# Kernel optimization log

Measured on AMD Instinct MI355X. Metric: run time of the kernel, lower is better.

The kernel has to match this reference:

```python
import jax, jax.numpy as jnp
import numpy as np

N, C, S = 16, 512, 4096

def setup_inputs() -> dict:
    rng = jax.random.key(0)
    k1, k2, k3 = jax.random.split(rng, 3)
    return {
        "key": jax.random.normal(k1, (N, C, S), dtype=jnp.float32),
        "value": jax.random.normal(k2, (N, C, S), dtype=jnp.float32),
        "query": jax.random.normal(k3, (N, C, S), dtype=jnp.float32),
    }

def reference(key, value, query):
    KC = key.shape[1]
    # query.permute(0,2,1): [N, C, S] -> [N, S, C]
    # sim_map = bmm(key, query^T): [N, C, C], scaled by KC^-0.5
    sim = jnp.einsum("ncs,nds->ncd", key, query) * (KC ** -0.5)
    # softmax over dim=1 (first C axis)
    sim = jax.nn.softmax(sim, axis=1)
    # context = bmm(sim, value): [N, C, C] @ [N, C, S] -> [N, C, S]
    context = jnp.einsum("ncd,nds->ncs", sim, value)
    return context
```

## Files before the change

### kernel.cpp

```cpp
#include <hip/hip_runtime.h>

typedef __bf16 bf16x8 __attribute__((ext_vector_type(8)));
typedef float f32x4 __attribute__((ext_vector_type(4)));
typedef unsigned short u16;
typedef u16 u16x4 __attribute__((ext_vector_type(4)));
typedef u16 u16x8 __attribute__((ext_vector_type(8)));

__device__ __forceinline__ u16 f2bf(float f) {
  unsigned u = __builtin_bit_cast(unsigned, f);
  unsigned r = (u + 0x7fffu + ((u >> 16) & 1u)) >> 16;
  return (u16)r;
}

__device__ __forceinline__ void gld_lds16(const u16* g, u16* l) {
  __builtin_amdgcn_global_load_lds(
      (__attribute__((address_space(1))) void*)(g),
      (__attribute__((address_space(3))) void*)(l), 16, 0, 0);
}

__device__ __forceinline__ f32x4 ntload4(const float* p) {
  return __builtin_nontemporal_load((const f32x4*)p);
}

__global__ __launch_bounds__(256) void k_cvt(const float* __restrict__ K,
                                             const float* __restrict__ Q,
                                             u16* __restrict__ Kb,
                                             u16* __restrict__ Qb) {
  const float* src = blockIdx.y ? Q : K;
  u16* dst = blockIdx.y ? Qb : Kb;
  const size_t i = (size_t)blockIdx.x * 2048 + threadIdx.x * 8;
  f32x4 a = ntload4(src + i);
  f32x4 b = ntload4(src + i + 4);
  u16x8 h;
  h[0] = f2bf(a[0]); h[1] = f2bf(a[1]); h[2] = f2bf(a[2]); h[3] = f2bf(a[3]);
  h[4] = f2bf(b[0]); h[5] = f2bf(b[1]); h[6] = f2bf(b[2]); h[7] = f2bf(b[3]);
  *(u16x8*)(dst + i) = h;
}

__global__ __launch_bounds__(512) void k_mix(const u16* __restrict__ Kb,
                                             const u16* __restrict__ Qb,
                                             float* __restrict__ Lp,
                                             const float* __restrict__ V,
                                             u16* __restrict__ Vt) {
  extern __shared__ char raw[];
  const int bid = blockIdx.x;
  const int t = threadIdx.x;

  if (bid % 5 == 0) {
    u16* sA = (u16*)raw;
    u16* sB = (u16*)(raw + 32768);
    const int sid0 = bid / 5;
    const int sid = (sid0 & 7) * 64 + (sid0 >> 3);
    const int n = sid >> 5;
    const int rem = sid & 31;
    const int kc = rem >> 4;
    const int r2 = rem & 15;
    const int cy = r2 >> 2, dx = r2 & 3;
    const int lane = t & 63, wid = t >> 6;
    const int wr = wid >> 2, wc = wid & 3;
    const float scale = 0.04419417382415922f;

    const u16* Ab = Kb + ((size_t)n * 512 + cy * 128) * 4096 + kc * 2048;
    const u16* Bb = Qb + ((size_t)n * 512 + dx * 128) * 4096 + kc * 2048;
    f32x4 acc[4][2] = {};
    const int srow0 = t >> 3;
    const int scol = ((t & 7) << 3) ^ ((srow0 & 7) << 3);

#define MIX_STAGE(buf, k0)                                                      \
  {                                                                             \
    _Pragma("unroll") for (int q = 0; q < 2; ++q) {                             \
      const int row = q * 64 + srow0;                                           \
      gld_lds16(Ab + (size_t)row * 4096 + (k0) + scol,                          \
                sA + (buf) * 8192 + (q * 512 + (wid << 6)) * 8);                \
      gld_lds16(Bb + (size_t)row * 4096 + (k0) + scol,                          \
                sB + (buf) * 8192 + (q * 512 + (wid << 6)) * 8);                \
    }                                                                           \
  }
#define MIX_COMPUTE(buf)                                                        \
  {                                                                             \
    _Pragma("unroll") for (int ki = 0; ki < 2; ++ki) {                          \
      bf16x8 a[4], b[2];                                                        \
      const int ce = ki * 32 + (lane >> 4) * 8;                                 \
      _Pragma("unroll") for (int mi = 0; mi < 4; ++mi) {                        \
        const int r = wr * 64 + mi * 16 + (lane & 15);                          \
        a[mi] = *(const bf16x8*)&sA[(buf) * 8192 + r * 64 + (ce ^ ((r & 7) << 3))]; \
      }                                                                         \
      _Pragma("unroll") for (int ni = 0; ni < 2; ++ni) {                        \
        const int r = wc * 32 + ni * 16 + (lane & 15);                          \
        b[ni] = *(const bf16x8*)&sB[(buf) * 8192 + r * 64 + (ce ^ ((r & 7) << 3))]; \
      }                                                                         \
      __builtin_amdgcn_s_setprio(1);                                            \
      _Pragma("unroll") for (int mi = 0; mi < 4; ++mi)                          \
        _Pragma("unroll") for (int ni = 0; ni < 2; ++ni)                        \
          acc[mi][ni] = __builtin_amdgcn_mfma_f32_16x16x32_bf16(                \
              a[mi], b[ni], acc[mi][ni], 0, 0, 0);                              \
      __builtin_amdgcn_s_setprio(0);                                            \
    }                                                                           \
  }

    MIX_STAGE(0, 0);
    __syncthreads();
    int cur = 0;
    for (int kt = 0; kt < 31; ++kt) {
      MIX_STAGE(cur ^ 1, (kt + 1) << 6);
      MIX_COMPUTE(cur);
      __syncthreads();
      cur ^= 1;
    }
    MIX_COMPUTE(cur);

    float* Lb = Lp + ((size_t)kc * 16 + n) * 512 * 512;
    const int c0 = cy * 128, d0 = dx * 128;
#pragma unroll
    for (int mi = 0; mi < 4; ++mi)
#pragma unroll
      for (int ni = 0; ni < 2; ++ni) {
        int colo = d0 + wc * 32 + ni * 16 + (lane & 15);
#pragma unroll
        for (int j = 0; j < 4; ++j) {
          int rowo = c0 + wr * 64 + mi * 16 + ((lane >> 4) << 2) + j;
          Lb[(size_t)rowo * 512 + colo] = acc[mi][ni][j] * scale;
        }
      }
#undef MIX_STAGE
#undef MIX_COMPUTE
  } else {
    const int vid = bid - bid / 5 - 1;
    const int sub = t >> 8, tt = t & 255;
    const int tile = vid * 2 + sub;
    const int n = tile >> 8;
    const int r = tile & 255;
    const int d0 = (r >> 6) * 128, s0 = (r & 63) * 64;
    float* lds = (float*)(raw + sub * 34816);
    {
      const int r0 = tt >> 4, c4 = (tt & 15) << 2;
#pragma unroll
      for (int p = 0; p < 8; ++p) {
        const int dr = r0 + p * 16;
        f32x4 v = ntload4(V + ((size_t)n * 512 + d0 + dr) * 4096 + s0 + c4);
        const int sw = ((dr >> 3) & 7) << 2;
        *(f32x4*)(&lds[dr * 68 + (c4 ^ sw)]) = v;
      }
    }
    __syncthreads();
    {
      const int sr0 = tt >> 4, dcol = (tt & 15) << 3;
#pragma unroll
      for (int p2 = 0; p2 < 4; ++p2) {
        const int sr = sr0 + p2 * 16;
        u16x8 h;
#pragma unroll
        for (int j = 0; j < 8; ++j) {
          const int d = dcol + j;
          h[j] = f2bf(lds[d * 68 + (sr ^ (((d >> 3) & 7) << 2))]);
        }
        *(u16x8*)(Vt + ((size_t)n * 4096 + s0 + sr) * 512 + d0 + dcol) = h;
      }
    }
  }
}

template <int KDIV>
__global__ __launch_bounds__(512) void k_stats2(const float* __restrict__ Lp,
                                                u16* __restrict__ E) {
  __shared__ f32x4 redm[16][32];
  __shared__ f32x4 reds[16][32];
  const int n = blockIdx.y;
  const int tx = threadIdx.x & 31, ty = threadIdx.x >> 5;
  const int d0 = blockIdx.x * 128 + tx * 4;
  const size_t CH = (size_t)16 * 512 * 512;
  const float* B = Lp + (size_t)n * 512 * 512 + d0;

  f32x4 m = {-3.0e38f, -3.0e38f, -3.0e38f, -3.0e38f};
  f32x4 s = {0.f, 0.f, 0.f, 0.f};
  for (int c = ty; c < 512; c += 16) {
    f32x4 v = *(const f32x4*)(B + (size_t)c * 512);
#pragma unroll
    for (int q = 1; q < KDIV; ++q) v += *(const f32x4*)(B + q * CH + (size_t)c * 512);
#pragma unroll
    for (int j = 0; j < 4; ++j) {
      float nm = fmaxf(m[j], v[j]);
      s[j] = s[j] * __expf(m[j] - nm) + __expf(v[j] - nm);
      m[j] = nm;
    }
  }
  redm[ty][tx] = m;
  reds[ty][tx] = s;
  __syncthreads();
  f32x4 M = redm[0][tx], S;
#pragma unroll
  for (int q = 1; q < 16; ++q)
#pragma unroll
    for (int j = 0; j < 4; ++j) M[j] = fmaxf(M[j], redm[q][tx][j]);
#pragma unroll
  for (int j = 0; j < 4; ++j) S[j] = 0.f;
#pragma unroll
  for (int q = 0; q < 16; ++q)
#pragma unroll
    for (int j = 0; j < 4; ++j) S[j] += reds[q][tx][j] * __expf(redm[q][tx][j] - M[j]);
  f32x4 si;
#pragma unroll
  for (int j = 0; j < 4; ++j) si[j] = 1.0f / S[j];

  u16* Eb = E + (size_t)n * 512 * 512 + d0;
  for (int c = ty; c < 512; c += 16) {
    f32x4 v = *(const f32x4*)(B + (size_t)c * 512);
#pragma unroll
    for (int q = 1; q < KDIV; ++q) v += *(const f32x4*)(B + q * CH + (size_t)c * 512);
    u16x4 h;
#pragma unroll
    for (int j = 0; j < 4; ++j) h[j] = f2bf(__expf(v[j] - M[j]) * si[j]);
    *(u16x4*)(Eb + (size_t)c * 512) = h;
  }
}

template <int KDIV>
__global__ __launch_bounds__(512) void k_simk(const u16* __restrict__ Kb,
                                              const u16* __restrict__ Qb,
                                              float* __restrict__ Lp) {
  __shared__ u16 sA[2][128 * 64];
  __shared__ u16 sB[2][128 * 64];
  constexpr int NB = 256 * KDIV;
  const int bid = blockIdx.x;
  const int sid = (bid & 7) * (NB / 8) + (bid >> 3);
  constexpr int PER_N = 16 * KDIV;
  const int n = sid / PER_N;
  const int rem = sid % PER_N;
  const int kc = rem >> 4;
  const int r2 = rem & 15;
  const int cy = r2 >> 2, dx = r2 & 3;
  const int t = threadIdx.x, lane = t & 63, wid = t >> 6;
  const int wr = wid >> 2, wc = wid & 3;
  const float scale = 0.04419417382415922f;

  const u16* Ab = Kb + ((size_t)n * 512 + cy * 128) * 4096 + kc * (4096 / KDIV);
  const u16* Bb = Qb + ((size_t)n * 512 + dx * 128) * 4096 + kc * (4096 / KDIV);
  f32x4 acc[4][2] = {};
  const int srow0 = t >> 3;
  const int scol = ((t & 7) << 3) ^ ((srow0 & 7) << 3);

#define SIM_STAGE(buf, k0)                                                      \
  {                                                                             \
    _Pragma("unroll") for (int q = 0; q < 2; ++q) {                             \
      const int row = q * 64 + srow0;                                           \
      gld_lds16(Ab + (size_t)row * 4096 + (k0) + scol,                          \
                &sA[buf][(q * 512 + (wid << 6)) * 8]);                          \
      gld_lds16(Bb + (size_t)row * 4096 + (k0) + scol,                          \
                &sB[buf][(q * 512 + (wid << 6)) * 8]);                          \
    }                                                                           \
  }
#define SIM_COMPUTE(buf)                                                        \
  {                                                                             \
    _Pragma("unroll") for (int ki = 0; ki < 2; ++ki) {                          \
      bf16x8 a[4], b[2];                                                        \
      const int ce = ki * 32 + (lane >> 4) * 8;                                 \
      _Pragma("unroll") for (int mi = 0; mi < 4; ++mi) {                        \
        const int r = wr * 64 + mi * 16 + (lane & 15);                          \
        a[mi] = *(const bf16x8*)&sA[buf][r * 64 + (ce ^ ((r & 7) << 3))];       \
      }                                                                         \
      _Pragma("unroll") for (int ni = 0; ni < 2; ++ni) {                        \
        const int r = wc * 32 + ni * 16 + (lane & 15);                          \
        b[ni] = *(const bf16x8*)&sB[buf][r * 64 + (ce ^ ((r & 7) << 3))];       \
      }                                                                         \
      _Pragma("unroll") for (int mi = 0; mi < 4; ++mi)                          \
        _Pragma("unroll") for (int ni = 0; ni < 2; ++ni)                        \
          acc[mi][ni] = __builtin_amdgcn_mfma_f32_16x16x32_bf16(                \
              a[mi], b[ni], acc[mi][ni], 0, 0, 0);                              \
    }                                                                           \
  }

  constexpr int NSTEP = 64 / KDIV;
  SIM_STAGE(0, 0);
  __syncthreads();
  int cur = 0;
  for (int kt = 0; kt < NSTEP - 1; ++kt) {
    SIM_STAGE(cur ^ 1, (kt + 1) << 6);
    SIM_COMPUTE(cur);
    __syncthreads();
    cur ^= 1;
  }
  SIM_COMPUTE(cur);

  float* Lb = Lp + ((size_t)kc * 16 + n) * 512 * 512;
  const int c0 = cy * 128, d0 = dx * 128;
#pragma unroll
  for (int mi = 0; mi < 4; ++mi)
#pragma unroll
    for (int ni = 0; ni < 2; ++ni) {
      int colo = d0 + wc * 32 + ni * 16 + (lane & 15);
#pragma unroll
      for (int j = 0; j < 4; ++j) {
        int rowo = c0 + wr * 64 + mi * 16 + ((lane >> 4) << 2) + j;
        Lb[(size_t)rowo * 512 + colo] = acc[mi][ni][j] * scale;
      }
    }
#undef SIM_STAGE
#undef SIM_COMPUTE
}

__global__ __launch_bounds__(256) void k_vt(const float* __restrict__ V,
                                            u16* __restrict__ Vt) {
  __shared__ float lds[128 * 68];
  const int n = blockIdx.z, d0 = blockIdx.y * 128, s0 = blockIdx.x * 64;
  const int t = threadIdx.x;
  {
    const int r0 = t >> 4, c4 = (t & 15) << 2;
#pragma unroll
    for (int p = 0; p < 8; ++p) {
      const int dr = r0 + p * 16;
      f32x4 v = ntload4(V + ((size_t)n * 512 + d0 + dr) * 4096 + s0 + c4);
      const int sw = ((dr >> 3) & 7) << 2;
      *(f32x4*)(&lds[dr * 68 + (c4 ^ sw)]) = v;
    }
  }
  __syncthreads();
  {
    const int sr0 = t >> 4, dcol = (t & 15) << 3;
#pragma unroll
    for (int p2 = 0; p2 < 4; ++p2) {
      const int sr = sr0 + p2 * 16;
      u16x8 h;
#pragma unroll
      for (int j = 0; j < 8; ++j) {
        const int d = dcol + j;
        h[j] = f2bf(lds[d * 68 + (sr ^ (((d >> 3) & 7) << 2))]);
      }
      *(u16x8*)(Vt + ((size_t)n * 4096 + s0 + sr) * 512 + d0 + dcol) = h;
    }
  }
}

__global__ __launch_bounds__(512) void k_ctx4(const u16* __restrict__ E,
                                              const u16* __restrict__ Vt,
                                              float* __restrict__ O) {
  __shared__ char lbuf[65536];
  u16* sA = (u16*)lbuf;
  u16* sB = (u16*)(lbuf + 32768);
  float* ldsf = (float*)lbuf;
  const int bid = blockIdx.x;
  const int sid = (bid & 7) * 256 + (bid >> 3);
  const int n = sid >> 7;
  const int rem = sid & 127;
  const int cy = rem >> 5, sx = rem & 31;
  const int t = threadIdx.x, lane = t & 63, wid = t >> 6;
  const int wr = wid >> 2, wc = wid & 3;

  const u16* Ab = E + ((size_t)n * 512 + cy * 128) * 512;
  const u16* Bb = Vt + ((size_t)n * 4096 + sx * 128) * 512;
  const int srow0 = t >> 3;
  const int scol = ((t & 7) << 3) ^ ((srow0 & 7) << 3);
  f32x4 acc[4][2] = {};

#define CTX_STAGE(buf, kd)                                                      \
  {                                                                             \
    _Pragma("unroll") for (int q = 0; q < 2; ++q) {                             \
      const int row = q * 64 + srow0;                                           \
      gld_lds16(Ab + (size_t)row * 512 + (kd) + scol,                           \
                sA + (buf) * 8192 + (q * 512 + (wid << 6)) * 8);                \
      gld_lds16(Bb + (size_t)row * 512 + (kd) + scol,                           \
                sB + (buf) * 8192 + (q * 512 + (wid << 6)) * 8);                \
    }                                                                           \
  }
#define CTX_COMPUTE(buf)                                                        \
  {                                                                             \
    _Pragma("unroll") for (int ki = 0; ki < 2; ++ki) {                          \
      bf16x8 a[4], b[2];                                                        \
      const int ce = ki * 32 + (lane >> 4) * 8;                                 \
      _Pragma("unroll") for (int mi = 0; mi < 4; ++mi) {                        \
        const int r = wr * 64 + mi * 16 + (lane & 15);                          \
        a[mi] = *(const bf16x8*)&sA[(buf) * 8192 + r * 64 + (ce ^ ((r & 7) << 3))]; \
      }                                                                         \
      _Pragma("unroll") for (int ni = 0; ni < 2; ++ni) {                        \
        const int r = wc * 32 + ni * 16 + (lane & 15);                          \
        b[ni] = *(const bf16x8*)&sB[(buf) * 8192 + r * 64 + (ce ^ ((r & 7) << 3))]; \
      }                                                                         \
      _Pragma("unroll") for (int mi = 0; mi < 4; ++mi)                          \
        _Pragma("unroll") for (int ni = 0; ni < 2; ++ni)                        \
          acc[mi][ni] = __builtin_amdgcn_mfma_f32_16x16x32_bf16(                \
              a[mi], b[ni], acc[mi][ni], 0, 0, 0);                              \
    }                                                                           \
  }

  CTX_STAGE(0, 0);
  __syncthreads();
  int cur = 0;
  for (int kt = 0; kt < 7; ++kt) {
    CTX_STAGE(cur ^ 1, (kt + 1) << 6);
    CTX_COMPUTE(cur);
    __syncthreads();
    cur ^= 1;
  }
  CTX_COMPUTE(cur);
  __syncthreads();

#pragma unroll
  for (int mi = 0; mi < 4; ++mi)
#pragma unroll
    for (int ni = 0; ni < 2; ++ni) {
      const int cl = wc * 32 + ni * 16 + (lane & 15);
#pragma unroll
      for (int j = 0; j < 4; ++j) {
        const int rl = wr * 64 + mi * 16 + ((lane >> 4) << 2) + j;
        ldsf[rl * 128 + (cl ^ (((rl >> 2) & 1) << 4))] = acc[mi][ni][j];
      }
    }
  __syncthreads();
  float* Ob = O + ((size_t)n * 512 + cy * 128) * 4096 + sx * 128;
#pragma unroll
  for (int p = 0; p < 8; ++p) {
    const int chunk = p * 512 + t;
    const int row = chunk >> 5;
    const int c4 = (chunk & 31) << 2;
    f32x4 v = *(const f32x4*)&ldsf[row * 128 + (c4 ^ (((row >> 2) & 1) << 4))];
    __builtin_nontemporal_store(v, (f32x4*)(Ob + (size_t)row * 4096 + c4));
  }
#undef CTX_STAGE
#undef CTX_COMPUTE
}

extern "C" void kernel_launch(void* const* d_in, const int* in_sizes, int n_in,
                              void* d_out, int out_size, void* d_ws, size_t ws_size,
                              hipStream_t stream) {
  const float* Kp = (const float*)d_in[0];
  const float* Vp = (const float*)d_in[1];
  const float* Qp = (const float*)d_in[2];
  float* Op = (float*)d_out;
  char* ws = (char*)d_ws;
  const size_t MB = 1024 * 1024;

  if (ws_size >= 192 * MB) {
    u16* Kb = (u16*)ws;
    u16* Qb = (u16*)(ws + 64 * MB);
    u16* Vt = (u16*)(ws + 128 * MB);
    u16* E  = (u16*)(ws + 64 * MB);
    float* Lp = Op;

    k_cvt<<<dim3(16384, 2), 256, 0, stream>>>(Kp, Qp, Kb, Qb);
    k_mix<<<2560, 512, 69632, stream>>>(Kb, Qb, Lp, Vp, Vt);
    k_stats2<2><<<dim3(4, 16), 512, 0, stream>>>(Lp, E);
    k_ctx4<<<2048, 512, 0, stream>>>(E, Vt, Op);
  } else if (ws_size >= 128 * MB) {
    u16* Kb = (u16*)ws;
    u16* Qb = (u16*)(ws + 64 * MB);
    u16* Vt = (u16*)ws;
    u16* E  = (u16*)(ws + 64 * MB);
    float* Lp = Op;

    k_cvt<<<dim3(16384, 2), 256, 0, stream>>>(Kp, Qp, Kb, Qb);
    k_simk<2><<<512, 512, 0, stream>>>(Kb, Qb, Lp);
    k_stats2<2><<<dim3(4, 16), 512, 0, stream>>>(Lp, E);
    k_vt<<<dim3(64, 4, 16), 256, 0, stream>>>(Vp, Vt);
    k_ctx4<<<2048, 512, 0, stream>>>(E, Vt, Op);
  }
}
```

Baseline: 220.9 us.

## Fuse Q fp32-to-bf16 conversion into the similarity GEMM B-tile loading

The separate conversion pass for Q is dropped. The similarity GEMM blocks now load fp32 Q tiles into registers, convert them to bf16 in flight and write them into swizzled LDS, while K still goes through the async global-to-LDS path. This removes one full fp32 read and bf16 write/read of Q through HBM, and shrinks the workspace needed for the fast path. In exchange the B-tile load goes through registers and adds an extra barrier per k-step. Each Q tile is also read in fp32 by the 4 cy tiles of each (n, kc) pair, so global read volume for Q may rise.

```diff
diff --git a/kernel.cpp b/kernel.cpp
--- a/kernel.cpp
+++ b/kernel.cpp
@@ -10,6 +10,13 @@
   unsigned u = __builtin_bit_cast(unsigned, f);
   unsigned r = (u + 0x7fffu + ((u >> 16) & 1u)) >> 16;
   return (u16)r;
+}
+
+__device__ __forceinline__ bf16x8 cvt8v(f32x4 a, f32x4 b) {
+  bf16x8 h;
+  h[0] = (__bf16)a[0]; h[1] = (__bf16)a[1]; h[2] = (__bf16)a[2]; h[3] = (__bf16)a[3];
+  h[4] = (__bf16)b[0]; h[5] = (__bf16)b[1]; h[6] = (__bf16)b[2]; h[7] = (__bf16)b[3];
+  return h;
 }
 
 __device__ __forceinline__ void gld_lds16(const u16* g, u16* l) {
@@ -37,11 +44,11 @@
   *(u16x8*)(dst + i) = h;
 }
 
-__global__ __launch_bounds__(512) void k_mix(const u16* __restrict__ Kb,
-                                             const u16* __restrict__ Qb,
-                                             float* __restrict__ Lp,
-                                             const float* __restrict__ V,
-                                             u16* __restrict__ Vt) {
+__global__ __launch_bounds__(512) void k_mix5(const u16* __restrict__ Kb,
+                                              const float* __restrict__ Q,
+                                              float* __restrict__ Lp,
+                                              const float* __restrict__ V,
+                                              u16* __restrict__ Vt) {
   extern __shared__ char raw[];
   const int bid = blockIdx.x;
   const int t = threadIdx.x;
@@ -61,20 +68,35 @@
     const float scale = 0.04419417382415922f;
 
     const u16* Ab = Kb + ((size_t)n * 512 + cy * 128) * 4096 + kc * 2048;
-    const u16* Bb = Qb + ((size_t)n * 512 + dx * 128) * 4096 + kc * 2048;
+    const float* Bq = Q + ((size_t)n * 512 + dx * 128) * 4096 + kc * 2048;
     f32x4 acc[4][2] = {};
     const int srow0 = t >> 3;
     const int scol = ((t & 7) << 3) ^ ((srow0 & 7) << 3);
-
-#define MIX_STAGE(buf, k0)                                                      \
+    const int br = t >> 2, bc = (t & 3) << 4;
+    const int bsw0 = bc ^ ((br & 7) << 3);
+    const int bsw1 = (bc + 8) ^ ((br & 7) << 3);
+    f32x4 qb[4];
+
+#define MIX_STAGE_A(buf, k0)                                                    \
   {                                                                             \
     _Pragma("unroll") for (int q = 0; q < 2; ++q) {                             \
       const int row = q * 64 + srow0;                                           \
       gld_lds16(Ab + (size_t)row * 4096 + (k0) + scol,                          \
                 sA + (buf) * 8192 + (q * 512 + (wid << 6)) * 8);                \
-      gld_lds16(Bb + (size_t)row * 4096 + (k0) + scol,                          \
-                sB + (buf) * 8192 + (q * 512 + (wid << 6)) * 8);                \
-    }                                                                           \
+    }                                                                           \
+  }
+#define MIX_LOAD_B(k0)                                                          \
+  {                                                                             \
+    const float* p = Bq + (size_t)br * 4096 + (k0) + bc;                        \
+    qb[0] = *(const f32x4*)p;                                                   \
+    qb[1] = *(const f32x4*)(p + 4);                                             \
+    qb[2] = *(const f32x4*)(p + 8);                                             \
+    qb[3] = *(const f32x4*)(p + 12);                                            \
+  }
+#define MIX_WRITE_B(buf)                                                        \
+  {                                                                             \
+    *(bf16x8*)&sB[(buf) * 8192 + br * 64 + bsw0] = cvt8v(qb[0], qb[1]);         \
+    *(bf16x8*)&sB[(buf) * 8192 + br * 64 + bsw1] = cvt8v(qb[2], qb[3]);         \
   }
 #define MIX_COMPUTE(buf)                                                        \
   {                                                                             \
@@ -98,16 +120,25 @@
     }                                                                           \
   }
 
-    MIX_STAGE(0, 0);
+    MIX_LOAD_B(0);
+    MIX_STAGE_A(0, 0);
+    MIX_WRITE_B(0);
     __syncthreads();
     int cur = 0;
-    for (int kt = 0; kt < 31; ++kt) {
-      MIX_STAGE(cur ^ 1, (kt + 1) << 6);
+#pragma unroll 1
+    for (int kt = 0; kt < 32; ++kt) {
+      if (kt < 31) {
+        MIX_STAGE_A(cur ^ 1, (kt + 1) << 6);
+        MIX_LOAD_B((kt + 1) << 6);
+      }
       MIX_COMPUTE(cur);
       __syncthreads();
+      if (kt < 31) {
+        MIX_WRITE_B(cur ^ 1);
+        __syncthreads();
+      }
       cur ^= 1;
     }
-    MIX_COMPUTE(cur);
 
     float* Lb = Lp + ((size_t)kc * 16 + n) * 512 * 512;
     const int c0 = cy * 128, d0 = dx * 128;
@@ -122,7 +153,9 @@
           Lb[(size_t)rowo * 512 + colo] = acc[mi][ni][j] * scale;
         }
       }
-#undef MIX_STAGE
+#undef MIX_STAGE_A
+#undef MIX_LOAD_B
+#undef MIX_WRITE_B
 #undef MIX_COMPUTE
   } else {
     const int vid = bid - bid / 5 - 1;
@@ -428,15 +461,14 @@
   char* ws = (char*)d_ws;
   const size_t MB = 1024 * 1024;
 
-  if (ws_size >= 192 * MB) {
+  if (ws_size >= 136 * MB) {
     u16* Kb = (u16*)ws;
-    u16* Qb = (u16*)(ws + 64 * MB);
-    u16* Vt = (u16*)(ws + 128 * MB);
-    u16* E  = (u16*)(ws + 64 * MB);
+    u16* Vt = (u16*)(ws + 64 * MB);
+    u16* E  = (u16*)(ws + 128 * MB);
     float* Lp = Op;
 
-    k_cvt<<<dim3(16384, 2), 256, 0, stream>>>(Kp, Qp, Kb, Qb);
-    k_mix<<<2560, 512, 69632, stream>>>(Kb, Qb, Lp, Vp, Vt);
+    k_cvt<<<dim3(16384, 1), 256, 0, stream>>>(Kp, Qp, Kb, nullptr);
+    k_mix5<<<2560, 512, 69632, stream>>>(Kb, Qp, Lp, Vp, Vt);
     k_stats2<2><<<dim3(4, 16), 512, 0, stream>>>(Lp, E);
     k_ctx4<<<2048, 512, 0, stream>>>(E, Vt, Op);
   } else if (ws_size >= 128 * MB) {
```

Result: slower. 237.2 us (+7.4%).
